# Kernel optimization log

Measured on AMD Instinct MI355X. Metric: run time of the kernel, lower is better.

Reference implementation:

```python
import jax, jax.numpy as jnp
import numpy as np

N_NODES = 50000
N_EDGES = 600000
IN_CH, HID, EMB = 128, 128, 64


def _glorot(key, shape):
    fan_in, fan_out = shape[1], shape[0]
    lim = np.sqrt(6.0 / (fan_in + fan_out))
    return jax.random.uniform(key, shape, jnp.float32, -lim, lim)


def setup_inputs() -> dict:
    key = jax.random.key(0)
    ks = jax.random.split(key, 12)
    x = jax.random.normal(ks[0], (N_NODES, IN_CH), jnp.float32)
    edge_index = jax.random.randint(ks[1], (2, N_EDGES), 0, N_NODES, jnp.int64)
    return {
        "x": x,
        "edge_index": edge_index,
        # SAGEConv layer 1: lin_l (neighbor, with bias) + lin_r (root, no bias)
        "w1n": _glorot(ks[2], (HID, IN_CH)),
        "w1r": _glorot(ks[3], (HID, IN_CH)),
        "b1": jnp.zeros((HID,), jnp.float32),
        "w2n": _glorot(ks[4], (HID, HID)),
        "w2r": _glorot(ks[5], (HID, HID)),
        "b2": jnp.zeros((HID,), jnp.float32),
        "w3n": _glorot(ks[6], (EMB, HID)),
        "w3r": _glorot(ks[7], (EMB, HID)),
        "b3": jnp.zeros((EMB,), jnp.float32),
    }


def _sage_conv(x, src, dst, wn, wr, b):
    # mean aggregation of source-node features at destination nodes
    msg = x[src]                                            # [E, d_in]
    agg = jax.ops.segment_sum(msg, dst, num_segments=N_NODES)
    deg = jax.ops.segment_sum(jnp.ones((src.shape[0],), x.dtype), dst,
                              num_segments=N_NODES)
    agg = agg / jnp.maximum(deg, 1.0)[:, None]
    return agg @ wn.T + x @ wr.T + b


def reference(x, edge_index, w1n, w1r, b1, w2n, w2r, b2, w3n, w3r, b3):
    src, dst = edge_index[0], edge_index[1]
    h = jax.nn.relu(_sage_conv(x, src, dst, w1n, w1r, b1))
    # dropout(p=0.3) is identity in inference mode
    h = jax.nn.relu(_sage_conv(h, src, dst, w2n, w2r, b2))
    h = _sage_conv(h, src, dst, w3n, w3r, b3)
    return h
```

## Files before the change

kernel.cpp:

```cpp
#include <hip/hip_runtime.h>
#include <hip/hip_bf16.h>

#define NN 50000
#define ZROW 50000
#define ELLW 64
#define F8MINDEG 6

#define NB 128
#define BSH 9
#define BCAP 8192
#define EPB 2048

typedef short bf16x8 __attribute__((ext_vector_type(8)));
typedef float f32x4 __attribute__((ext_vector_type(4)));
typedef float floatx2 __attribute__((ext_vector_type(2)));

#if __has_builtin(__builtin_amdgcn_cvt_pk_f32_fp8) && __has_builtin(__builtin_amdgcn_cvt_pk_fp8_f32)
#define HWF8 1
#endif

__device__ __forceinline__ float bf_lo(unsigned int p) {
    union { unsigned int u; float f; } c; c.u = p << 16; return c.f;
}
__device__ __forceinline__ float bf_hi(unsigned int p) {
    union { unsigned int u; float f; } c; c.u = p & 0xffff0000u; return c.f;
}
__device__ __forceinline__ unsigned short bfbits(float f) {
    __hip_bfloat16 h = __float2bfloat16(f);
    union { __hip_bfloat16 b; unsigned short s; } c; c.b = h; return c.s;
}
__device__ __forceinline__ unsigned int pack_bf(float a, float b) {
    return (unsigned int)bfbits(a) | ((unsigned int)bfbits(b) << 16);
}
__device__ __forceinline__ void stv(float* p, float v) { *p = v; }
__device__ __forceinline__ void stv(unsigned short* p, float v) { *p = bfbits(v); }

__device__ __forceinline__ floatx2 bfpair(unsigned int p) {
    union { unsigned int u; float f; } lo, hi;
    lo.u = p << 16; hi.u = p & 0xffff0000u;
    return floatx2{lo.f, hi.f};
}
__device__ __forceinline__ void acc8v(const uint4& u, floatx2* a) {
    a[0] += bfpair(u.x); a[1] += bfpair(u.y);
    a[2] += bfpair(u.z); a[3] += bfpair(u.w);
}

__device__ __forceinline__ unsigned int enc1(float f) {
#ifdef HWF8
    return (unsigned int)__builtin_amdgcn_cvt_pk_fp8_f32(f, f, 0, false) & 0xffu;
#else
    union { float f; unsigned u; } c; c.f = f;
    unsigned s = (c.u >> 24) & 0x80u;
    float af = fabsf(f);
    if (af >= 448.f) return s | 0x7eu;
    if (af < 0.0078125f) {
        unsigned m = (unsigned)(af * 512.f + 0.5f);
        return s | (m > 7u ? 7u : m);
    }
    unsigned u = c.u & 0x7fffffffu;
    u += 0x7ffffu + ((u >> 20) & 1u);
    int e = (int)(u >> 23) - 120;
    if (e < 1) { unsigned m = (unsigned)(af * 512.f + 0.5f); return s | (m > 7u ? 7u : m); }
    if (e > 15) return s | 0x7eu;
    return s | ((unsigned)e << 3) | ((u >> 20) & 7u);
#endif
}
__device__ __forceinline__ unsigned int packf8_4(float x, float y, float z, float w) {
#ifdef HWF8
    int u = __builtin_amdgcn_cvt_pk_fp8_f32(x, y, 0, false);
    u = __builtin_amdgcn_cvt_pk_fp8_f32(z, w, u, true);
    return (unsigned int)u;
#else
    return enc1(x) | (enc1(y) << 8) | (enc1(z) << 16) | (enc1(w) << 24);
#endif
}
__device__ __forceinline__ void accf8v(const uint4& u, floatx2* a) {
#ifdef HWF8
    a[0] += __builtin_amdgcn_cvt_pk_f32_fp8(u.x, false);
    a[1] += __builtin_amdgcn_cvt_pk_f32_fp8(u.x, true);
    a[2] += __builtin_amdgcn_cvt_pk_f32_fp8(u.y, false);
    a[3] += __builtin_amdgcn_cvt_pk_f32_fp8(u.y, true);
    a[4] += __builtin_amdgcn_cvt_pk_f32_fp8(u.z, false);
    a[5] += __builtin_amdgcn_cvt_pk_f32_fp8(u.z, true);
    a[6] += __builtin_amdgcn_cvt_pk_f32_fp8(u.w, false);
    a[7] += __builtin_amdgcn_cvt_pk_f32_fp8(u.w, true);
#else
    const unsigned ww[4] = {u.x, u.y, u.z, u.w};
#pragma unroll
    for (int k = 0; k < 4; k++) {
#pragma unroll
        for (int j = 0; j < 4; j++) {
            unsigned b = (ww[k] >> (8 * j)) & 0xffu;
            unsigned v = ((b & 0x80u) << 24) | (((b & 0x7fu) + (120u << 3)) << 20);
            if ((b & 0x78u) == 0) v = 0u;
            union { unsigned u; float f; } c; c.u = v;
            a[(k * 4 + j) >> 1][(k * 4 + j) & 1] += c.f;
        }
    }
#endif
}

__global__ __launch_bounds__(256) void wb3z_kernel(
    const float* __restrict__ w1n, const float* __restrict__ w1r,
    const float* __restrict__ w2n, const float* __restrict__ w2r,
    const float* __restrict__ w3n, const float* __restrict__ w3r,
    unsigned short* __restrict__ wB1, unsigned short* __restrict__ wB2,
    unsigned short* __restrict__ wB3, int* __restrict__ zblk,
    unsigned short* __restrict__ xb, unsigned short* __restrict__ axc,
    unsigned short* __restrict__ h1b,
    unsigned char* __restrict__ xf8, unsigned char* __restrict__ h1f8) {
    int i = blockIdx.x * blockDim.x + threadIdx.x;
    if (i < 2048) zblk[i] = 0;
    int p = i - 2048;
    if (p >= 0 && p < 256) {
        if (p < 64)       ((unsigned int*)(xb  + (size_t)ZROW * 128))[p] = 0u;
        else if (p < 128) ((unsigned int*)(axc + (size_t)ZROW * 128))[p - 64] = 0u;
        else if (p < 192) ((unsigned int*)(h1b + (size_t)ZROW * 128))[p - 128] = 0u;
        else if (p < 224) ((unsigned int*)(xf8 + (size_t)ZROW * 128))[p - 192] = 0u;
        else              ((unsigned int*)(h1f8 + (size_t)ZROW * 128))[p - 224] = 0u;
    }
    if (i >= 12288) return;
    if (i < 8192) {
        const float* wn = (i < 4096) ? w1n : w2n;
        const float* wr = (i < 4096) ? w1r : w2r;
        unsigned short* wB = (i < 4096) ? wB1 : wB2;
        int li = i & 4095;
        int row = li >> 5;
        int j = (li & 31) * 4;
        float4 a = *(const float4*)(wn + (size_t)row * 128 + j);
        float4 b = *(const float4*)(wr + (size_t)row * 128 + j);
        *(uint2*)(wB + (size_t)row * 256 + j) = uint2{pack_bf(a.x, a.y), pack_bf(a.z, a.w)};
        *(uint2*)(wB + (size_t)row * 256 + 128 + j) = uint2{pack_bf(b.x, b.y), pack_bf(b.z, b.w)};
    } else {
        int li = i - 8192;
        const float* w = (li < 2048) ? w3n : w3r;
        int rbase = (li < 2048) ? 0 : 64;
        int lj = li & 2047;
        int row = lj >> 5;
        int j = (lj & 31) * 4;
        float4 a = *(const float4*)(w + (size_t)row * 128 + j);
        *(uint2*)(wB3 + (size_t)(rbase + row) * 128 + j) =
            uint2{pack_bf(a.x, a.y), pack_bf(a.z, a.w)};
    }
}

__global__ __launch_bounds__(256) void binify_cvt_kernel(
    const float* __restrict__ x,
    unsigned short* __restrict__ xb,
    unsigned char* __restrict__ xf8,
    const int* __restrict__ src,
    const int* __restrict__ dst,
    unsigned int* __restrict__ bpos,
    unsigned int* __restrict__ barr,
    int n4, int E, int nEB) {
    __shared__ int cnt[NB];
    __shared__ int gbase[NB];
    const int t = threadIdx.x;
    const int blk = blockIdx.x;
    if (blk < nEB) {
        int e0 = blk * EPB;
        int ss[8], dd[8], rr[8];
        bool v[8];
#pragma unroll
        for (int k = 0; k < 8; k++) {
            int e = e0 + t + (k << 8);
            v[k] = (e < E);
            ss[k] = v[k] ? src[e] : 0;
            dd[k] = v[k] ? dst[e] : 0;
            rr[k] = 0;
        }
        if (t < NB) cnt[t] = 0;
        __syncthreads();
#pragma unroll
        for (int k = 0; k < 8; k++)
            if (v[k]) rr[k] = atomicAdd(&cnt[dd[k] >> BSH], 1);
        __syncthreads();
        if (t < NB) {
            int c = cnt[t];
            gbase[t] = c ? (int)atomicAdd(&bpos[t], (unsigned)c) : 0;
        }
        __syncthreads();
#pragma unroll
        for (int k = 0; k < 8; k++) {
            if (v[k]) {
                int b = dd[k] >> BSH;
                int pos = gbase[b] + rr[k];
                if (pos < BCAP)
                    barr[b * BCAP + pos] =
                        (unsigned)ss[k] | ((unsigned)dd[k] << 16);
            }
        }
    }
    int gtid = blk * 256 + t;
    int gs = gridDim.x << 8;
    for (int i = gtid; i < n4; i += gs) {
        float4 vv = *(const float4*)(x + 4 * (size_t)i);
        *(uint2*)(xb + 4 * (size_t)i) = uint2{pack_bf(vv.x, vv.y), pack_bf(vv.z, vv.w)};
        *(unsigned int*)(xf8 + 4 * (size_t)i) = packf8_4(vv.x, vv.y, vv.z, vv.w);
    }
}

__global__ __launch_bounds__(256) void ellbuild_kernel(
    const unsigned int* __restrict__ bpos,
    const unsigned int* __restrict__ barr,
    unsigned short* __restrict__ ell,
    int* __restrict__ cnt) {
    __shared__ alignas(16) unsigned short lell[512 * 64];
    __shared__ int lcnt[512];
    const int t = threadIdx.x;
    const int b = blockIdx.x;
    const unsigned PADP = 0xC350C350u;
    for (int i = t; i < 4096; i += 256) ((uint4*)lell)[i] = uint4{PADP, PADP, PADP, PADP};
    for (int i = t; i < 512; i += 256) lcnt[i] = 0;
    __syncthreads();
    int ne = (int)bpos[b];
    if (ne > BCAP) ne = BCAP;
    const unsigned int* seg = barr + (size_t)b * BCAP;
    for (int i = t; i < ne; i += 256) {
        unsigned p = seg[i];
        int ln = (p >> 16) & 511;
        int r = atomicAdd(&lcnt[ln], 1);
        lell[(ln << 6) + (r & (ELLW - 1))] = (unsigned short)(p & 0xffffu);
    }
    __syncthreads();
    int node0 = b << BSH;
    int nn = NN - node0;
    if (nn > 512) nn = 512;
    if (nn <= 0) return;
    uint4* gell = (uint4*)(ell + (size_t)node0 * ELLW);
    const uint4* sell = (const uint4*)lell;
    for (int i = t; i < nn * 8; i += 256) gell[i] = sell[i];
    for (int i = t; i < nn; i += 256) cnt[node0 + i] = lcnt[i];
}

template <bool F8>
__global__ __launch_bounds__(512) void fused_layer(
    const int* __restrict__ cnt, const unsigned short* __restrict__ ell,
    const unsigned char* __restrict__ hf8,
    const unsigned short* __restrict__ hb,
    const unsigned short* __restrict__ B,
    const float* __restrict__ bias,
    unsigned short* __restrict__ outb,
    unsigned char* __restrict__ outf8,
    int M) {
    __shared__ unsigned short AsG[2][128 * 72];
    __shared__ unsigned short Bs[2][128 * 72];
    const int t = threadIdx.x;
    const int w = t >> 6, l = t & 63;
    const int lr = l & 15, lq = l >> 4;
    const int m0 = blockIdx.x * 128;

#pragma unroll
    for (int j = 0; j < 2; j++) {
        int c = t + j * 512;
        int row = c >> 3;
        int ko = (c & 7) * 8;
        *(uint4*)(&Bs[0][row * 72 + ko]) = *(const uint4*)(B + (size_t)row * 256 + ko);
    }

#pragma unroll
    for (int p = 0; p < 2; p++) {
        int r = p * 64 + (t >> 3);
        int n = m0 + r;
        int ch = (t & 7) << 4;
        int deg = (n < NN) ? cnt[n] : 0;
        int dd8 = (min(deg, ELLW) + 7) & ~7;
        const unsigned short* cl = ell + (size_t)n * ELLW;
        floatx2 a[8];
#pragma unroll
        for (int k = 0; k < 8; k++) a[k] = floatx2{0.f, 0.f};
        if (deg >= F8MINDEG) {
            for (int i = 0; i < dd8; i += 8) {
                uint4 idv = *(const uint4*)(cl + i);
                int i0 = idv.x & 0xffff, i1 = idv.x >> 16;
                int i2 = idv.y & 0xffff, i3 = idv.y >> 16;
                int i4 = idv.z & 0xffff, i5 = idv.z >> 16;
                int i6 = idv.w & 0xffff, i7 = idv.w >> 16;
                uint4 u0 = *(const uint4*)(hf8 + (size_t)i0 * 128 + ch);
                uint4 u1 = *(const uint4*)(hf8 + (size_t)i1 * 128 + ch);
                uint4 u2 = *(const uint4*)(hf8 + (size_t)i2 * 128 + ch);
                uint4 u3 = *(const uint4*)(hf8 + (size_t)i3 * 128 + ch);
                uint4 u4 = *(const uint4*)(hf8 + (size_t)i4 * 128 + ch);
                uint4 u5 = *(const uint4*)(hf8 + (size_t)i5 * 128 + ch);
                uint4 u6 = *(const uint4*)(hf8 + (size_t)i6 * 128 + ch);
                uint4 u7 = *(const uint4*)(hf8 + (size_t)i7 * 128 + ch);
                accf8v(u0, a); accf8v(u1, a); accf8v(u2, a); accf8v(u3, a);
                accf8v(u4, a); accf8v(u5, a); accf8v(u6, a); accf8v(u7, a);
            }
        } else if (deg > 0) {
            for (int i = 0; i < dd8; i += 8) {
                uint4 idv = *(const uint4*)(cl + i);
                int is[8];
                is[0] = idv.x & 0xffff; is[1] = idv.x >> 16;
                is[2] = idv.y & 0xffff; is[3] = idv.y >> 16;
                is[4] = idv.z & 0xffff; is[5] = idv.z >> 16;
                is[6] = idv.w & 0xffff; is[7] = idv.w >> 16;
#pragma unroll
                for (int k = 0; k < 8; k++) {
                    uint4 lo = *(const uint4*)(hb + (size_t)is[k] * 128 + ch);
                    uint4 hi = *(const uint4*)(hb + (size_t)is[k] * 128 + ch + 8);
                    acc8v(lo, a); acc8v(hi, a + 4);
                }
            }
        }
        float s = 1.0f / (float)max(deg, 1);
        uint4 p0 = {pack_bf(a[0][0] * s, a[0][1] * s), pack_bf(a[1][0] * s, a[1][1] * s),
                    pack_bf(a[2][0] * s, a[2][1] * s), pack_bf(a[3][0] * s, a[3][1] * s)};
        uint4 p1 = {pack_bf(a[4][0] * s, a[4][1] * s), pack_bf(a[5][0] * s, a[5][1] * s),
                    pack_bf(a[6][0] * s, a[6][1] * s), pack_bf(a[7][0] * s, a[7][1] * s)};
        int slab = (t & 7) >> 2;
        int ck = ((t & 7) & 3) << 4;
        *(uint4*)(&AsG[slab][r * 72 + ck]) = p0;
        *(uint4*)(&AsG[slab][r * 72 + ck + 8]) = p1;
    }
    __syncthreads();

    f32x4 acc[8];
#pragma unroll
    for (int tn = 0; tn < 8; tn++) acc[tn] = f32x4{0.f, 0.f, 0.f, 0.f};
    const int arow = w * 16 + lr;
    const size_t groot = (size_t)min(m0 + arow, ZROW) * 128;

#pragma unroll
    for (int ks = 0; ks < 4; ks++) {
        uint4 pfB[2];
        if (ks < 3) {
#pragma unroll
            for (int j = 0; j < 2; j++) {
                int c = t + j * 512;
                int row = c >> 3;
                int ko = (c & 7) * 8;
                pfB[j] = *(const uint4*)(B + (size_t)row * 256 + (ks + 1) * 64 + ko);
            }
        }
        const unsigned short* bs = Bs[ks & 1];
#pragma unroll
        for (int kc = 0; kc < 2; kc++) {
            int lk = kc * 32 + lq * 8;
            bf16x8 af, bfr[8];
            if (ks < 2) af = *(const bf16x8*)(&AsG[ks][arow * 72 + lk]);
            else        af = *(const bf16x8*)(hb + groot + (ks - 2) * 64 + lk);
#pragma unroll
            for (int tn = 0; tn < 8; tn++)
                bfr[tn] = *(const bf16x8*)(&bs[(tn * 16 + lr) * 72 + lk]);
#pragma unroll
            for (int tn = 0; tn < 8; tn++)
                acc[tn] = __builtin_amdgcn_mfma_f32_16x16x32_bf16(
                    af, bfr[tn], acc[tn], 0, 0, 0);
        }
        if (ks < 3) {
#pragma unroll
            for (int j = 0; j < 2; j++) {
                int c = t + j * 512;
                int row = c >> 3;
                int ko = (c & 7) * 8;
                *(uint4*)(&Bs[(ks + 1) & 1][row * 72 + ko]) = pfB[j];
            }
            __syncthreads();
        }
    }

#pragma unroll
    for (int tn = 0; tn < 8; tn++) {
        int n = tn * 16 + lr;
        float bj = bias[n];
#pragma unroll
        for (int i = 0; i < 4; i++) {
            int m = m0 + w * 16 + lq * 4 + i;
            if (m < M) {
                float v = fmaxf(acc[tn][i] + bj, 0.f);
                stv(&outb[(size_t)m * 128 + n], v);
                if (F8) outf8[(size_t)m * 128 + n] = (unsigned char)enc1(v);
            }
        }
    }
}

__global__ __launch_bounds__(256) void gather_add_kernel(
    const int* __restrict__ cnt, const unsigned short* __restrict__ ell,
    const unsigned short* __restrict__ tu,
    const float* __restrict__ b3,
    float* __restrict__ out, int n_nodes) {
    int tid = blockIdx.x * blockDim.x + threadIdx.x;
    int n = tid >> 3;
    if (n >= n_nodes) return;
    int c = (tid & 7) << 3;
    int deg = cnt[n];
    int dd8 = (min(deg, ELLW) + 7) & ~7;
    const unsigned short* cl = ell + (size_t)n * ELLW;
    floatx2 a[4];
#pragma unroll
    for (int k = 0; k < 4; k++) a[k] = floatx2{0.f, 0.f};
    for (int i = 0; i < dd8; i += 8) {
        uint4 idv = *(const uint4*)(cl + i);
        int i0 = idv.x & 0xffff, i1 = idv.x >> 16;
        int i2 = idv.y & 0xffff, i3 = idv.y >> 16;
        int i4 = idv.z & 0xffff, i5 = idv.z >> 16;
        int i6 = idv.w & 0xffff, i7 = idv.w >> 16;
        uint4 u0 = *(const uint4*)(tu + (size_t)i0 * 128 + c);
        uint4 u1 = *(const uint4*)(tu + (size_t)i1 * 128 + c);
        uint4 u2 = *(const uint4*)(tu + (size_t)i2 * 128 + c);
        uint4 u3 = *(const uint4*)(tu + (size_t)i3 * 128 + c);
        uint4 u4 = *(const uint4*)(tu + (size_t)i4 * 128 + c);
        uint4 u5 = *(const uint4*)(tu + (size_t)i5 * 128 + c);
        uint4 u6 = *(const uint4*)(tu + (size_t)i6 * 128 + c);
        uint4 u7 = *(const uint4*)(tu + (size_t)i7 * 128 + c);
        acc8v(u0, a); acc8v(u1, a); acc8v(u2, a); acc8v(u3, a);
        acc8v(u4, a); acc8v(u5, a); acc8v(u6, a); acc8v(u7, a);
    }
    float s = 1.0f / (float)max(deg, 1);
    uint4 uu = *(const uint4*)(tu + (size_t)n * 128 + 64 + c);
    float4 bA = *(const float4*)(b3 + c);
    float4 bB = *(const float4*)(b3 + c + 4);
    float* o = out + (size_t)n * 64 + c;
    o[0] = a[0][0] * s + bf_lo(uu.x) + bA.x;
    o[1] = a[0][1] * s + bf_hi(uu.x) + bA.y;
    o[2] = a[1][0] * s + bf_lo(uu.y) + bA.z;
    o[3] = a[1][1] * s + bf_hi(uu.y) + bA.w;
    o[4] = a[2][0] * s + bf_lo(uu.z) + bB.x;
    o[5] = a[2][1] * s + bf_hi(uu.z) + bB.y;
    o[6] = a[3][0] * s + bf_lo(uu.w) + bB.z;
    o[7] = a[3][1] * s + bf_hi(uu.w) + bB.w;
}

template <int NKS, bool RELU, bool BIAS, typename OUT_T>
__global__ __launch_bounds__(256) void mfma_gemm(
    const unsigned short* __restrict__ A0, const unsigned short* __restrict__ A1,
    const unsigned short* __restrict__ B,
    const float* __restrict__ bias,
    OUT_T* __restrict__ out,
    int M) {
    constexpr int KTOT = NKS * 64;
    __shared__ unsigned short As[2][128 * 72];
    __shared__ unsigned short Bs[2][128 * 72];
    const int t = threadIdx.x;
    const int w = t >> 6, l = t & 63;
    const int m0 = blockIdx.x * 128;
    const int lr = l & 15, lq = l >> 4;

#pragma unroll
    for (int j = 0; j < 4; j++) {
        int c = t + j * 256;
        int row = c >> 3;
        int ko = (c & 7) * 8;
        int gm = m0 + row;
        uint4 va = {0u, 0u, 0u, 0u};
        if (gm < M) va = *(const uint4*)(A0 + (size_t)gm * 128 + ko);
        *(uint4*)(&As[0][row * 72 + ko]) = va;
        *(uint4*)(&Bs[0][row * 72 + ko]) = *(const uint4*)(B + (size_t)row * KTOT + ko);
    }
    __syncthreads();

    f32x4 acc[2][8];
#pragma unroll
    for (int tm = 0; tm < 2; tm++)
#pragma unroll
        for (int tn = 0; tn < 8; tn++) acc[tm][tn] = f32x4{0.f, 0.f, 0.f, 0.f};

#pragma unroll
    for (int ks = 0; ks < NKS; ks++) {
        uint4 pfA[4], pfB[4];
        if (ks + 1 < NKS) {
            int ns = ks + 1;
            const unsigned short* Asrc = (ns < NKS / 2)
                ? (A0 + (size_t)ns * 64) : (A1 + (size_t)(ns - NKS / 2) * 64);
#pragma unroll
            for (int j = 0; j < 4; j++) {
                int c = t + j * 256;
                int row = c >> 3;
                int ko = (c & 7) * 8;
                int gm = m0 + row;
                pfA[j] = uint4{0u, 0u, 0u, 0u};
                if (gm < M) pfA[j] = *(const uint4*)(Asrc + (size_t)gm * 128 + ko);
                pfB[j] = *(const uint4*)(B + (size_t)row * KTOT + ns * 64 + ko);
            }
        }
        const unsigned short* as = As[ks & 1];
        const unsigned short* bs = Bs[ks & 1];
#pragma unroll
        for (int kc = 0; kc < 2; kc++) {
            int lk = kc * 32 + lq * 8;
            bf16x8 af[2], bfr[8];
            af[0] = *(const bf16x8*)(&as[(w * 32 + lr) * 72 + lk]);
            af[1] = *(const bf16x8*)(&as[(w * 32 + 16 + lr) * 72 + lk]);
#pragma unroll
            for (int tn = 0; tn < 8; tn++)
                bfr[tn] = *(const bf16x8*)(&bs[(tn * 16 + lr) * 72 + lk]);
#pragma unroll
            for (int tm = 0; tm < 2; tm++)
#pragma unroll
                for (int tn = 0; tn < 8; tn++)
                    acc[tm][tn] = __builtin_amdgcn_mfma_f32_16x16x32_bf16(
                        af[tm], bfr[tn], acc[tm][tn], 0, 0, 0);
        }
        if (ks + 1 < NKS) {
#pragma unroll
            for (int j = 0; j < 4; j++) {
                int c = t + j * 256;
                int row = c >> 3;
                int ko = (c & 7) * 8;
                *(uint4*)(&As[(ks + 1) & 1][row * 72 + ko]) = pfA[j];
                *(uint4*)(&Bs[(ks + 1) & 1][row * 72 + ko]) = pfB[j];
            }
            __syncthreads();
        }
    }

#pragma unroll
    for (int tn = 0; tn < 8; tn++) {
        int n = tn * 16 + lr;
        float bj = BIAS ? bias[n] : 0.f;
#pragma unroll
        for (int tm = 0; tm < 2; tm++) {
#pragma unroll
            for (int i = 0; i < 4; i++) {
                int m = m0 + w * 32 + tm * 16 + lq * 4 + i;
                if (m < M) {
                    float v = acc[tm][tn][i] + bj;
                    if (RELU) v = fmaxf(v, 0.f);
                    stv(&out[(size_t)m * 128 + n], v);
                }
            }
        }
    }
}

extern "C" void kernel_launch(void* const* d_in, const int* in_sizes, int n_in,
                              void* d_out, int out_size, void* d_ws, size_t ws_size,
                              hipStream_t stream) {
    const float* x  = (const float*)d_in[0];
    const int* ei   = (const int*)d_in[1];
    const float* w1n = (const float*)d_in[2];
    const float* w1r = (const float*)d_in[3];
    const float* b1  = (const float*)d_in[4];
    const float* w2n = (const float*)d_in[5];
    const float* w2r = (const float*)d_in[6];
    const float* b2  = (const float*)d_in[7];
    const float* w3n = (const float*)d_in[8];
    const float* w3r = (const float*)d_in[9];
    const float* b3  = (const float*)d_in[10];
    float* out = (float*)d_out;

    const int E = in_sizes[1] / 2;
    const int* src = ei;
    const int* dst = ei + E;

    char* ws = (char*)d_ws;
    unsigned short* xb  = (unsigned short*)(ws);
    unsigned short* axc = (unsigned short*)(ws + 13000000);
    unsigned short* h1b = (unsigned short*)(ws + 26000000);
    unsigned short* h2b = (unsigned short*)(ws + 39000000);
    unsigned int* barr  = (unsigned int*)(ws + 39000000);
    unsigned short* ell = (unsigned short*)(ws + 52000000);
    int* cnt            = (int*)  (ws + 64800000);
    int* zblk           = (int*)  (ws + 65400000);
    unsigned int* bpos  = (unsigned int*)(zblk + 1536);
    unsigned short* wB1 = (unsigned short*)(ws + 65500000);
    unsigned short* wB2 = (unsigned short*)(ws + 65600000);
    unsigned short* wB3 = (unsigned short*)(ws + 65700000);
    unsigned char* xf8  = (unsigned char*)(ws + 65800000);
    unsigned char* h1f8 = (unsigned char*)(ws + 72300000);

    const int nEB = (E + EPB - 1) / EPB;

    wb3z_kernel<<<48, 256, 0, stream>>>(
        w1n, w1r, w2n, w2r, w3n, w3r, wB1, wB2, wB3, zblk, xb, axc, h1b, xf8, h1f8);
    binify_cvt_kernel<<<2048, 256, 0, stream>>>(x, xb, xf8, src, dst,
                                                bpos, barr, NN * 32, E, nEB);
    ellbuild_kernel<<<(NN + 511) / 512, 256, 0, stream>>>(bpos, barr, ell, cnt);

    const int mTiles = (NN + 127) / 128;

    fused_layer<true><<<mTiles, 512, 0, stream>>>(
        cnt, ell, xf8, xb, wB1, b1, h1b, h1f8, NN);

    fused_layer<false><<<mTiles, 512, 0, stream>>>(
        cnt, ell, h1f8, h1b, wB2, b2, h2b, nullptr, NN);

    mfma_gemm<2, false, false, unsigned short>
        <<<mTiles, 256, 0, stream>>>(h2b, h2b + 64, wB3, nullptr, axc, NN);
    gather_add_kernel<<<(NN * 8 + 255) / 256, 256, 0, stream>>>(
        cnt, ell, axc, b3, out, NN);
}
```

Measured before the change: 201.7 us.

## Fuse layer-3 projection GEMM into layer-2 fused kernel epilogue

Layer 2's activated output tile is staged in shared memory as bf16, and the layer-3 weight matrix is multiplied in the same kernel, writing the projected features straight to the gather buffer. This removes the separate mfma_gemm launch and the h2 write/read round trip through global memory. The cost is extra LDS traffic, a few more barriers, and more registers in the fused kernel, which may reduce occupancy.

```diff
diff --git a/kernel.cpp b/kernel.cpp
--- a/kernel.cpp
+++ b/kernel.cpp
@@ -233,12 +233,13 @@
     for (int i = t; i < nn; i += 256) cnt[node0 + i] = lcnt[i];
 }
 
-template <bool F8>
+template <bool F8, bool L3T>
 __global__ __launch_bounds__(512) void fused_layer(
     const int* __restrict__ cnt, const unsigned short* __restrict__ ell,
     const unsigned char* __restrict__ hf8,
     const unsigned short* __restrict__ hb,
     const unsigned short* __restrict__ B,
+    const unsigned short* __restrict__ B3,
     const float* __restrict__ bias,
     unsigned short* __restrict__ outb,
     unsigned char* __restrict__ outf8,
@@ -360,6 +361,8 @@
         }
     }
 
+    unsigned short* h2s = &AsG[0][0];
+    unsigned short* B3s = &Bs[0][0];
 #pragma unroll
     for (int tn = 0; tn < 8; tn++) {
         int n = tn * 16 + lr;
@@ -367,10 +370,51 @@
 #pragma unroll
         for (int i = 0; i < 4; i++) {
             int m = m0 + w * 16 + lq * 4 + i;
-            if (m < M) {
-                float v = fmaxf(acc[tn][i] + bj, 0.f);
+            float v = fmaxf(acc[tn][i] + bj, 0.f);
+            if (L3T) {
+                int r = w * 16 + lq * 4 + i;
+                h2s[r * 136 + n] = (m < M) ? bfbits(v) : (unsigned short)0;
+            } else if (m < M) {
                 stv(&outb[(size_t)m * 128 + n], v);
                 if (F8) outf8[(size_t)m * 128 + n] = (unsigned char)enc1(v);
+            }
+        }
+    }
+
+    if (L3T) {
+        __syncthreads();
+        for (int c = t; c < 2048; c += 512) {
+            int row = c >> 4;
+            int ko = (c & 15) * 8;
+            *(uint4*)(&B3s[row * 136 + ko]) = *(const uint4*)(B3 + (size_t)row * 128 + ko);
+        }
+        __syncthreads();
+        f32x4 acc3[8];
+#pragma unroll
+        for (int tn = 0; tn < 8; tn++) acc3[tn] = f32x4{0.f, 0.f, 0.f, 0.f};
+#pragma unroll
+        for (int ks3 = 0; ks3 < 2; ks3++) {
+#pragma unroll
+            for (int kc = 0; kc < 2; kc++) {
+                int lk3 = ks3 * 64 + kc * 32 + lq * 8;
+                bf16x8 af = *(const bf16x8*)(&h2s[(w * 16 + lr) * 136 + lk3]);
+                bf16x8 bfr[8];
+#pragma unroll
+                for (int tn = 0; tn < 8; tn++)
+                    bfr[tn] = *(const bf16x8*)(&B3s[(tn * 16 + lr) * 136 + lk3]);
+#pragma unroll
+                for (int tn = 0; tn < 8; tn++)
+                    acc3[tn] = __builtin_amdgcn_mfma_f32_16x16x32_bf16(
+                        af, bfr[tn], acc3[tn], 0, 0, 0);
+            }
+        }
+#pragma unroll
+        for (int tn = 0; tn < 8; tn++) {
+            int n = tn * 16 + lr;
+#pragma unroll
+            for (int i = 0; i < 4; i++) {
+                int m = m0 + w * 16 + lq * 4 + i;
+                if (m < M) stv(&outb[(size_t)m * 128 + n], acc3[tn][i]);
             }
         }
     }
@@ -423,108 +467,6 @@
     o[7] = a[3][1] * s + bf_hi(uu.w) + bB.w;
 }
 
-template <int NKS, bool RELU, bool BIAS, typename OUT_T>
-__global__ __launch_bounds__(256) void mfma_gemm(
-    const unsigned short* __restrict__ A0, const unsigned short* __restrict__ A1,
-    const unsigned short* __restrict__ B,
-    const float* __restrict__ bias,
-    OUT_T* __restrict__ out,
-    int M) {
-    constexpr int KTOT = NKS * 64;
-    __shared__ unsigned short As[2][128 * 72];
-    __shared__ unsigned short Bs[2][128 * 72];
-    const int t = threadIdx.x;
-    const int w = t >> 6, l = t & 63;
-    const int m0 = blockIdx.x * 128;
-    const int lr = l & 15, lq = l >> 4;
-
-#pragma unroll
-    for (int j = 0; j < 4; j++) {
-        int c = t + j * 256;
-        int row = c >> 3;
-        int ko = (c & 7) * 8;
-        int gm = m0 + row;
-        uint4 va = {0u, 0u, 0u, 0u};
-        if (gm < M) va = *(const uint4*)(A0 + (size_t)gm * 128 + ko);
-        *(uint4*)(&As[0][row * 72 + ko]) = va;
-        *(uint4*)(&Bs[0][row * 72 + ko]) = *(const uint4*)(B + (size_t)row * KTOT + ko);
-    }
-    __syncthreads();
-
-    f32x4 acc[2][8];
-#pragma unroll
-    for (int tm = 0; tm < 2; tm++)
-#pragma unroll
-        for (int tn = 0; tn < 8; tn++) acc[tm][tn] = f32x4{0.f, 0.f, 0.f, 0.f};
-
-#pragma unroll
-    for (int ks = 0; ks < NKS; ks++) {
-        uint4 pfA[4], pfB[4];
-        if (ks + 1 < NKS) {
-            int ns = ks + 1;
-            const unsigned short* Asrc = (ns < NKS / 2)
-                ? (A0 + (size_t)ns * 64) : (A1 + (size_t)(ns - NKS / 2) * 64);
-#pragma unroll
-            for (int j = 0; j < 4; j++) {
-                int c = t + j * 256;
-                int row = c >> 3;
-                int ko = (c & 7) * 8;
-                int gm = m0 + row;
-                pfA[j] = uint4{0u, 0u, 0u, 0u};
-                if (gm < M) pfA[j] = *(const uint4*)(Asrc + (size_t)gm * 128 + ko);
-                pfB[j] = *(const uint4*)(B + (size_t)row * KTOT + ns * 64 + ko);
-            }
-        }
-        const unsigned short* as = As[ks & 1];
-        const unsigned short* bs = Bs[ks & 1];
-#pragma unroll
-        for (int kc = 0; kc < 2; kc++) {
-            int lk = kc * 32 + lq * 8;
-            bf16x8 af[2], bfr[8];
-            af[0] = *(const bf16x8*)(&as[(w * 32 + lr) * 72 + lk]);
-            af[1] = *(const bf16x8*)(&as[(w * 32 + 16 + lr) * 72 + lk]);
-#pragma unroll
-            for (int tn = 0; tn < 8; tn++)
-                bfr[tn] = *(const bf16x8*)(&bs[(tn * 16 + lr) * 72 + lk]);
-#pragma unroll
-            for (int tm = 0; tm < 2; tm++)
-#pragma unroll
-                for (int tn = 0; tn < 8; tn++)
-                    acc[tm][tn] = __builtin_amdgcn_mfma_f32_16x16x32_bf16(
-                        af[tm], bfr[tn], acc[tm][tn], 0, 0, 0);
-        }
-        if (ks + 1 < NKS) {
-#pragma unroll
-            for (int j = 0; j < 4; j++) {
-                int c = t + j * 256;
-                int row = c >> 3;
-                int ko = (c & 7) * 8;
-                *(uint4*)(&As[(ks + 1) & 1][row * 72 + ko]) = pfA[j];
-                *(uint4*)(&Bs[(ks + 1) & 1][row * 72 + ko]) = pfB[j];
-            }
-            __syncthreads();
-        }
-    }
-
-#pragma unroll
-    for (int tn = 0; tn < 8; tn++) {
-        int n = tn * 16 + lr;
-        float bj = BIAS ? bias[n] : 0.f;
-#pragma unroll
-        for (int tm = 0; tm < 2; tm++) {
-#pragma unroll
-            for (int i = 0; i < 4; i++) {
-                int m = m0 + w * 32 + tm * 16 + lq * 4 + i;
-                if (m < M) {
-                    float v = acc[tm][tn][i] + bj;
-                    if (RELU) v = fmaxf(v, 0.f);
-                    stv(&out[(size_t)m * 128 + n], v);
-                }
-            }
-        }
-    }
-}
-
 extern "C" void kernel_launch(void* const* d_in, const int* in_sizes, int n_in,
                               void* d_out, int out_size, void* d_ws, size_t ws_size,
                               hipStream_t stream) {
@@ -549,7 +491,6 @@
     unsigned short* xb  = (unsigned short*)(ws);
     unsigned short* axc = (unsigned short*)(ws + 13000000);
     unsigned short* h1b = (unsigned short*)(ws + 26000000);
-    unsigned short* h2b = (unsigned short*)(ws + 39000000);
     unsigned int* barr  = (unsigned int*)(ws + 39000000);
     unsigned short* ell = (unsigned short*)(ws + 52000000);
     int* cnt            = (int*)  (ws + 64800000);
@@ -571,14 +512,12 @@
 
     const int mTiles = (NN + 127) / 128;
 
-    fused_layer<true><<<mTiles, 512, 0, stream>>>(
-        cnt, ell, xf8, xb, wB1, b1, h1b, h1f8, NN);
-
-    fused_layer<false><<<mTiles, 512, 0, stream>>>(
-        cnt, ell, h1f8, h1b, wB2, b2, h2b, nullptr, NN);
-
-    mfma_gemm<2, false, false, unsigned short>
-        <<<mTiles, 256, 0, stream>>>(h2b, h2b + 64, wB3, nullptr, axc, NN);
+    fused_layer<true, false><<<mTiles, 512, 0, stream>>>(
+        cnt, ell, xf8, xb, wB1, nullptr, b1, h1b, h1f8, NN);
+
+    fused_layer<false, true><<<mTiles, 512, 0, stream>>>(
+        cnt, ell, h1f8, h1b, wB2, wB3, b2, axc, nullptr, NN);
+
     gather_add_kernel<<<(NN * 8 + 255) / 256, 256, 0, stream>>>(
         cnt, ell, axc, b3, out, NN);
 }
```

New measurement: 193.1 us (median of 2 runs). 4.3% less time.
